# Performance work log

Measured on AMD Instinct MI355X. Metric: run time of the kernel, lower is better.

Reference implementation:

```python
import jax, jax.numpy as jnp
import numpy as np

B = 65536
NE = 256   # n_encode
NH = 256   # n_hidden
NC = 4     # n_command
D = 64     # n_depth (BatchNorm channels)
F = 32     # n_features
M = D * (F // 2)  # 1024
EPS = 1e-5


def setup_inputs() -> dict:
    key = jax.random.key(0)
    ks = jax.random.split(key, 8)
    s = 0.05
    return {
        "feature": jax.random.normal(ks[0], (B, NE), jnp.float32),
        "hidden":  jax.random.normal(ks[1], (B, NH), jnp.float32),
        "command": jax.random.normal(ks[2], (B, NC), jnp.float32),
        # linear weights (torch Linear stores [out, in]); xavier-like scale
        "Wq":  jax.random.normal(ks[3], (D, NC), jnp.float32) * s,
        "Wkz": jax.random.normal(ks[4], (M, NE), jnp.float32) * s,
        "Wkh": jax.random.normal(ks[5], (M, NH), jnp.float32) * s,
        "Wvz": jax.random.normal(ks[6], (M, NE), jnp.float32) * s,
        "Wvh": jax.random.normal(ks[7], (M, NH), jnp.float32) * s,
        # BatchNorm1d(64) affine params (normV exists in __init__ but is unused)
        "gammaQ": jnp.ones((D,), jnp.float32),
        "betaQ":  jnp.zeros((D,), jnp.float32),
        "gammaK": jnp.ones((D,), jnp.float32),
        "betaK":  jnp.zeros((D,), jnp.float32),
    }


def reference(feature, hidden, command, Wq, Wkz, Wkh, Wvz, Wvh,
              gammaQ, betaQ, gammaK, betaK):
    # Q projection: [B, D]; BatchNorm1d over batch (training-mode batch stats,
    # biased variance, matching torch).
    Q = command @ Wq.T
    mQ = jnp.mean(Q, axis=0)
    vQ = jnp.mean(jnp.square(Q - mQ), axis=0)
    Qn = (Q - mQ) / jnp.sqrt(vQ + EPS) * gammaQ + betaQ          # [B, D]

    # K: cat([B,M],[B,M]) -> [B, 2M] -> view [B, F, D] -> transpose -> [B, D, F]
    K = jnp.concatenate([feature @ Wkz.T, hidden @ Wkh.T], axis=1)
    K = K.reshape(-1, F, D).transpose(0, 2, 1)                    # [B, D, F]
    mK = jnp.mean(K, axis=(0, 2), keepdims=True)
    vK = jnp.mean(jnp.square(K - mK), axis=(0, 2), keepdims=True)
    Kn = (K - mK) / jnp.sqrt(vK + EPS) * gammaK[None, :, None] + betaK[None, :, None]

    # V: [B, F, D], NOT batch-normed (normV is dead code in the original)
    V = jnp.concatenate([feature @ Wvz.T, hidden @ Wvh.T], axis=1).reshape(-1, F, D)

    # attention: [B,1,D] @ [B,D,F] -> [B,F] scores; softmax over F; then @ V
    A = jax.nn.softmax(jnp.einsum('bd,bdf->bf', Qn, Kn) / np.sqrt(D).astype(np.float32), axis=-1)
    s = jnp.einsum('bf,bfd->bd', A, V)                            # [B, D]
    return s
```

## Files before the change

kernel.cpp:

```cpp
#include <hip/hip_runtime.h>
#include <hip/hip_bf16.h>
#include <math.h>


typedef float  f32x4   __attribute__((ext_vector_type(4)));
typedef float  f32x16  __attribute__((ext_vector_type(16)));
typedef __bf16 bf16x4  __attribute__((ext_vector_type(4)));
typedef __bf16 bf16x8  __attribute__((ext_vector_type(8)));

#define MFMA16(A, B, C) __builtin_amdgcn_mfma_f32_16x16x32_bf16((A), (B), (C), 0, 0, 0)
#define MFMA32(A, B, C) __builtin_amdgcn_mfma_f32_32x32x16_bf16((A), (B), (C), 0, 0, 0)

#define EPSV 1e-5f

#define WS_WV    0x000000u
#define WS_WKF   0x100000u
#define WS_G     0x120000u
#define WS_CS    0x1A0000u
#define WS_CMDP  0x1A0800u
#define WS_T     0x1A1800u
#define WS_U     0x1A3800u
#define WS_WQ2   0x1A5800u
#define WS_C0    0x1A5C00u

__device__ __forceinline__ void gl_lds16(const void* g, void* l)
{
    __builtin_amdgcn_global_load_lds(
        (const __attribute__((address_space(1))) unsigned int*)g,
        (__attribute__((address_space(3))) unsigned int*)l, 16, 0, 0);
}

__global__ __launch_bounds__(512, 2) void setup1(const float* __restrict__ feat,
        const float* __restrict__ hid, const float4* __restrict__ cmd,
        const float* __restrict__ Wvz, const float* __restrict__ Wvh,
        __bf16* __restrict__ WV, float* __restrict__ CMDP, float* __restrict__ CS,
        __bf16* __restrict__ Gp)
{
    __shared__ __bf16 T[2 * 256 * 40];
    __shared__ float sm[8][14];
    const int blk = blockIdx.x;
    const int tid = threadIdx.x;

    if (blk >= 384) {
        const int b2 = blk - 384;
        float v[14];
#pragma unroll
        for (int k = 0; k < 14; ++k) v[k] = 0.f;
#pragma unroll
        for (int i = 0; i < 4; ++i) {
            float4 c = cmd[(b2 * 4 + i) * 512 + tid];
            v[0] += c.x;  v[1] += c.y;  v[2] += c.z;  v[3] += c.w;
            v[4] += c.x*c.x; v[5] += c.x*c.y; v[6] += c.x*c.z; v[7] += c.x*c.w;
            v[8] += c.y*c.y; v[9] += c.y*c.z; v[10] += c.y*c.w;
            v[11] += c.z*c.z; v[12] += c.z*c.w; v[13] += c.w*c.w;
        }
#pragma unroll
        for (int k = 0; k < 14; ++k) {
            float s = v[k];
#pragma unroll
            for (int off = 32; off; off >>= 1) s += __shfl_xor(s, off);
            if ((tid & 63) == 0) sm[tid >> 6][k] = s;
        }
        __syncthreads();
        if (tid < 14) {
            float s = 0.f;
#pragma unroll
            for (int w = 0; w < 8; ++w) s += sm[w][tid];
            CMDP[b2 * 14 + tid] = s;
        }
        return;
    }
    if (blk >= 128) {
        int t = (blk - 128) * 512 + tid;
        int e = t * 4;
        const float* src = (e < 262144) ? (Wvz + e) : (Wvh + (e - 262144));
        float4 a = *(const float4*)src;
        bf16x4 vv = { (__bf16)a.x, (__bf16)a.y, (__bf16)a.z, (__bf16)a.w };
        *(bf16x4*)(WV + e) = vv;
        return;
    }

    const int mat  = blk >> 6;
    const int chunk = blk & 63;
    const float* X = mat ? hid : feat;
    float* cs = CS + mat * 256;
    const int k0   = chunk * 1024;
    const int wid  = tid >> 6, lane = tid & 63, quad = lane >> 4, l15 = lane & 15;
    const int c    = tid & 255;
    const int t8   = tid >> 8;

    f32x4 acc[2][16];
#pragma unroll
    for (int mt = 0; mt < 2; ++mt)
#pragma unroll
        for (int nt = 0; nt < 16; ++nt) acc[mt][nt] = (f32x4){0.f, 0.f, 0.f, 0.f};

    const float* Xc = X + (size_t)k0 * 256 + c;
    float ra[16], rb[16];
    float clsum = 0.f;

#define GRAM_LOAD(R, IT) do { \
        const float* p_ = Xc + (size_t)(IT) * 32 * 256; \
        _Pragma("unroll") \
        for (int i_ = 0; i_ < 16; ++i_) (R)[i_] = p_[(size_t)(t8 + 2 * i_) * 256]; \
    } while (0)
#define GRAM_WRITE(R, BUFO) do { \
        _Pragma("unroll") \
        for (int i_ = 0; i_ < 16; ++i_) { \
            float x_ = (R)[i_]; clsum += x_; \
            T[(BUFO) + c * 40 + t8 + 2 * i_] = (__bf16)x_; } \
    } while (0)
#define GRAM_MFMA(BUFO) do { \
        const __bf16* Tb_ = &T[(BUFO)]; \
        bf16x8 a0_ = *(const bf16x8*)&Tb_[(wid * 32 +      l15) * 40 + quad * 8]; \
        bf16x8 a1_ = *(const bf16x8*)&Tb_[(wid * 32 + 16 + l15) * 40 + quad * 8]; \
        _Pragma("unroll") \
        for (int nt_ = 0; nt_ < 16; ++nt_) { \
            bf16x8 b_ = *(const bf16x8*)&Tb_[(nt_ * 16 + l15) * 40 + quad * 8]; \
            acc[0][nt_] = MFMA16(a0_, b_, acc[0][nt_]); \
            acc[1][nt_] = MFMA16(a1_, b_, acc[1][nt_]); } \
    } while (0)

    GRAM_LOAD(ra, 0);
    GRAM_LOAD(rb, 1);
    GRAM_WRITE(ra, 0);
    GRAM_LOAD(ra, 2);
    __syncthreads();

    for (int it2 = 0; it2 < 16; ++it2) {
        GRAM_WRITE(rb, 10240);
        if (it2 < 15) GRAM_LOAD(rb, 2 * it2 + 3);
        GRAM_MFMA(0);
        __syncthreads();
        if (it2 < 15) {
            GRAM_WRITE(ra, 0);
            if (it2 < 14) GRAM_LOAD(ra, 2 * it2 + 4);
        }
        GRAM_MFMA(10240);
        __syncthreads();
    }
#undef GRAM_LOAD
#undef GRAM_WRITE
#undef GRAM_MFMA

    atomicAdd(&cs[c], clsum);
    __bf16* outp = Gp + (size_t)blk * 65536;
#pragma unroll
    for (int mt = 0; mt < 2; ++mt)
#pragma unroll
        for (int nt = 0; nt < 16; ++nt)
#pragma unroll
            for (int r = 0; r < 4; ++r) {
                int gi = wid * 32 + mt * 16 + quad * 4 + r;
                int gj = nt * 16 + l15;
                outp[gi * 256 + gj] = (__bf16)acc[mt][nt][r];
            }
}

__global__ void gram_reduce(const __bf16* __restrict__ Gp, float* __restrict__ G)
{
    int o = blockIdx.x * 256 + threadIdx.x;
    int mat = o >> 16, e = o & 65535;
    const __bf16* p = Gp + (size_t)mat * 64 * 65536 + e;
    float s = 0.f;
#pragma unroll 8
    for (int c = 0; c < 64; ++c) s += (float)p[(size_t)c * 65536];
    G[o] = s;
}

__global__ void rowstats(const float* __restrict__ Wkz, const float* __restrict__ Wkh,
        const float* __restrict__ G, const float* __restrict__ CS,
        float* __restrict__ Tout, float* __restrict__ Uout)
{
    const int blk = blockIdx.x;
    const int mat = blk >> 7, jg = blk & 127;
    const float* Wsrc = (mat ? Wkh : Wkz) + (size_t)jg * 8 * 256;
    const float* Gm = G + (size_t)mat * 65536;
    const float* cs = CS + mat * 256;
    __shared__ float wlT[256 * 8];
    __shared__ float red[4][16];
    const int tid = threadIdx.x, wid = tid >> 6, lane = tid & 63;
#pragma unroll
    for (int jj = 0; jj < 8; ++jj) wlT[tid * 8 + jj] = Wsrc[jj * 256 + tid];
    __syncthreads();
    float inner[8];
#pragma unroll
    for (int jj = 0; jj < 8; ++jj) inner[jj] = 0.f;
    for (int r = 0; r < 256; ++r) {
        float g = Gm[r * 256 + tid];
        float4 w0 = *(const float4*)&wlT[r * 8];
        float4 w1 = *(const float4*)&wlT[r * 8 + 4];
        inner[0] = fmaf(w0.x, g, inner[0]); inner[1] = fmaf(w0.y, g, inner[1]);
        inner[2] = fmaf(w0.z, g, inner[2]); inner[3] = fmaf(w0.w, g, inner[3]);
        inner[4] = fmaf(w1.x, g, inner[4]); inner[5] = fmaf(w1.y, g, inner[5]);
        inner[6] = fmaf(w1.z, g, inner[6]); inner[7] = fmaf(w1.w, g, inner[7]);
    }
    float cst = cs[tid];
#pragma unroll
    for (int jj = 0; jj < 8; ++jj) {
        float wme = wlT[tid * 8 + jj];
        float p = wme * inner[jj];
        float u = wme * cst;
#pragma unroll
        for (int off = 32; off; off >>= 1) { p += __shfl_xor(p, off); u += __shfl_xor(u, off); }
        if (lane == 0) { red[wid][jj] = p; red[wid][jj + 8] = u; }
    }
    __syncthreads();
    if (tid < 16) {
        float s = red[0][tid] + red[1][tid] + red[2][tid] + red[3][tid];
        int jj = tid & 7;
        int j = mat * 1024 + jg * 8 + jj;
        if (tid < 8) Tout[j] = s; else Uout[j] = s;
    }
}

__global__ void finalize_kernel(const float* __restrict__ Wq,
        const float* __restrict__ gQ, const float* __restrict__ bQ,
        const float* __restrict__ gK, const float* __restrict__ bK,
        const float* __restrict__ CMDP, const float* __restrict__ T,
        const float* __restrict__ U, float* __restrict__ Wq2, float* __restrict__ C0)
{
    __shared__ float s14[14];
    const int d = threadIdx.x;
    if (d < 14) {
        float s = 0.f;
        for (int b = 0; b < 32; ++b) s += CMDP[b * 14 + d];
        s14[d] = s;
    }
    __syncthreads();
    float s4[4] = { s14[0], s14[1], s14[2], s14[3] };
    float gc[4][4];
    gc[0][0] = s14[4];
    gc[0][1] = gc[1][0] = s14[5];
    gc[0][2] = gc[2][0] = s14[6];
    gc[0][3] = gc[3][0] = s14[7];
    gc[1][1] = s14[8];
    gc[1][2] = gc[2][1] = s14[9];
    gc[1][3] = gc[3][1] = s14[10];
    gc[2][2] = s14[11];
    gc[2][3] = gc[3][2] = s14[12];
    gc[3][3] = s14[13];
    float wq[4];
#pragma unroll
    for (int c = 0; c < 4; ++c) wq[c] = Wq[d * 4 + c];
    const float invB = 1.0f / 65536.0f;
    float mQ = (wq[0]*s4[0] + wq[1]*s4[1] + wq[2]*s4[2] + wq[3]*s4[3]) * invB;
    float eq2 = 0.f;
#pragma unroll
    for (int c = 0; c < 4; ++c)
#pragma unroll
        for (int c2 = 0; c2 < 4; ++c2) eq2 += wq[c] * wq[c2] * gc[c][c2];
    eq2 *= invB;
    float vQ  = eq2 - mQ * mQ;
    float aQ  = gQ[d] / sqrtf(vQ + EPSV);
    float bQv = bQ[d] - mQ * aQ;
    float S2 = 0.f, S1 = 0.f;
#pragma unroll
    for (int f = 0; f < 32; ++f) { S2 += T[f * 64 + d]; S1 += U[f * 64 + d]; }
    const float invBF = 1.0f / (65536.0f * 32.0f);
    float e2 = S2 * invBF, mK = S1 * invBF;
    float vK = e2 - mK * mK;
    float aK = gK[d] / sqrtf(vK + EPSV);
    float c1 = aQ * aK * 0.125f;
    C0[d] = bQv * aK * 0.125f;
#pragma unroll
    for (int c = 0; c < 4; ++c) Wq2[d * 4 + c] = c1 * wq[c];
}

__global__ void foldK(const float* __restrict__ Wkz, const float* __restrict__ Wkh,
                      const float* __restrict__ Wq2, const float* __restrict__ C0,
                      __bf16* __restrict__ WKF)
{
    const int blk = blockIdx.x;
    const int h = blk / 96, rr = blk % 96;
    const int k = threadIdx.x;
    float s = 0.f;
    if (rr < 80) {
        const int c = rr >> 4, fl = rr & 15;
        const float* Wsrc = (h ? Wkh : Wkz) + (size_t)fl * 64 * 256;
        for (int d = 0; d < 64; ++d) {
            float coef = (c == 0) ? C0[d] : Wq2[d * 4 + (c - 1)];
            s = fmaf(coef, Wsrc[d * 256 + k], s);
        }
    }
    WKF[(size_t)(h * 96 + rr) * 256 + k] = (__bf16)s;
}

__global__ __launch_bounds__(256, 2) void fused_attn(
        const float* __restrict__ feat, const float* __restrict__ hid,
        const float4* __restrict__ cmd, const __bf16* __restrict__ WV,
        const __bf16* __restrict__ WKF, float* __restrict__ out)
{
    __shared__ __bf16 BUF[32768];
    __shared__ __bf16 WGTs[16 * 132];
    const int tid  = threadIdx.x;
    const int wid  = tid >> 6, lane = tid & 63;
    const int l5   = lane & 31, hi = lane >> 5;
    const int fl   = l5 & 15;
    const bool low = (l5 < 16);
    const int wrow = (blockIdx.x << 7) + (wid << 5);

#define STAGE_CHUNK(SRC, DSTBASE, I) do { \
        int n_ = (wid << 1) + ((I) << 3) + hi; \
        gl_lds16((SRC) + n_ * 256 + ((l5 ^ (n_ & 31)) << 3), \
                 &BUF[(DSTBASE) + (((wid << 1) + ((I) << 3)) << 8)]); \
    } while (0)

    float l_i[16];
    f32x16 s_acc[2];
#pragma unroll
    for (int r = 0; r < 16; ++r) { l_i[r] = 0.f; s_acc[0][r] = 0.f; s_acc[1][r] = 0.f; }

    for (int h = 0; h < 2; ++h) {
        const float* X = h ? hid : feat;
        const __bf16* Wkf = WKF + ((size_t)h * 96 << 8);

        bf16x8 a2[16];
#pragma unroll
        for (int u = 0; u < 16; ++u) {
            const float* p = X + ((size_t)(wrow + l5) << 8) + u * 16 + hi * 8;
            float4 x0 = *(const float4*)p;
            float4 x1 = *(const float4*)(p + 4);
            a2[u] = (bf16x8){ (__bf16)x0.x, (__bf16)x0.y, (__bf16)x0.z, (__bf16)x0.w,
                              (__bf16)x1.x, (__bf16)x1.y, (__bf16)x1.z, (__bf16)x1.w };
        }

        __syncthreads();
#pragma unroll
        for (int i = 0; i < 12; ++i)
            STAGE_CHUNK(Wkf, 0, i);
        __syncthreads();

        f32x16 acc1[3];
#pragma unroll
        for (int nt = 0; nt < 3; ++nt)
#pragma unroll
            for (int r = 0; r < 16; ++r) acc1[nt][r] = 0.f;
        __builtin_amdgcn_s_setprio(1);
#pragma unroll
        for (int ks = 0; ks < 16; ++ks)
#pragma unroll
            for (int nt = 0; nt < 3; ++nt) {
                int n = nt * 32 + l5;
                bf16x8 b = *(const bf16x8*)&BUF[n * 256 + (((ks * 2 + hi) ^ (n & 31)) << 3)];
                acc1[nt] = MFMA32(a2[ks], b, acc1[nt]);
            }
        __builtin_amdgcn_s_setprio(0);

#pragma unroll
        for (int g = 0; g < 4; ++g) {
            bf16x4 wv4;
#pragma unroll
            for (int j = 0; j < 4; ++j) {
                const int r = g * 4 + j;
                const int row32 = j + 8 * g + 4 * hi;
                float4 cm = cmd[wrow + row32];
                float e0, e1, t0[3], t1[3];
#pragma unroll
                for (int nt = 0; nt < 3; ++nt) {
                    e0 = acc1[nt][r];
                    e1 = __shfl_xor(e0, 16);
                    t0[nt] = low ? e0 : e1;
                    t1[nt] = low ? e1 : e0;
                }
                float sc = t0[0] + cm.x * t1[0] + cm.y * t0[1]
                                 + cm.z * t1[1] + cm.w * t0[2];
                float w = __expf(sc);
                wv4[j] = (__bf16)w;
                float ws = w;
                ws += __shfl_xor(ws, 1); ws += __shfl_xor(ws, 2);
                ws += __shfl_xor(ws, 4); ws += __shfl_xor(ws, 8);
                l_i[r] += ws;
            }
            if (low) *(bf16x4*)&WGTs[fl * 132 + (wid << 5) + 8 * g + 4 * hi] = wv4;
        }

        __syncthreads();

        {
            const __bf16* base = WV + ((size_t)(h * 16) << 14);
#pragma unroll
            for (int i = 0; i < 8; ++i)
                STAGE_CHUNK(base, 0, i);
        }

        for (int f2 = 0; f2 < 16; ++f2) {
            const int bufsel = (f2 & 1) << 14;
            __syncthreads();
            if (f2 < 15) {
                const __bf16* base = WV + ((size_t)(h * 16 + f2 + 1) << 14);
                const int nsel = bufsel ^ 16384;
#pragma unroll
                for (int i = 0; i < 8; ++i)
                    STAGE_CHUNK(base, nsel, i);
            }
            __builtin_amdgcn_sched_barrier(0);
            f32x16 acc2[2];
#pragma unroll
            for (int r = 0; r < 16; ++r) { acc2[0][r] = 0.f; acc2[1][r] = 0.f; }
            __builtin_amdgcn_s_setprio(1);
#pragma unroll
            for (int ks = 0; ks < 16; ++ks)
#pragma unroll
                for (int nt = 0; nt < 2; ++nt) {
                    int n = nt * 32 + l5;
                    bf16x8 b = *(const bf16x8*)&BUF[bufsel + n * 256
                                                    + (((ks * 2 + hi) ^ (n & 31)) << 3)];
                    acc2[nt] = MFMA32(a2[ks], b, acc2[nt]);
                }
            __builtin_amdgcn_s_setprio(0);
#pragma unroll
            for (int g = 0; g < 4; ++g) {
                bf16x4 wv = *(const bf16x4*)&WGTs[f2 * 132 + (wid << 5) + 8 * g + 4 * hi];
#pragma unroll
                for (int j = 0; j < 4; ++j) {
                    float w = (float)wv[j];
                    s_acc[0][g * 4 + j] += w * acc2[0][g * 4 + j];
                    s_acc[1][g * 4 + j] += w * acc2[1][g * 4 + j];
                }
            }
        }
    }
#undef STAGE_CHUNK

#pragma unroll
    for (int g = 0; g < 4; ++g)
#pragma unroll
        for (int j = 0; j < 4; ++j) {
            const int r = g * 4 + j;
            float inv = 1.0f / l_i[r];
            size_t row = (size_t)(wrow + j + 8 * g + 4 * hi);
            out[(row << 6) + l5]      = s_acc[0][r] * inv;
            out[(row << 6) + 32 + l5] = s_acc[1][r] * inv;
        }
}

extern "C" void kernel_launch(void* const* d_in, const int* in_sizes, int n_in,
                              void* d_out, int out_size, void* d_ws, size_t ws_size,
                              hipStream_t stream)
{
    (void)in_sizes; (void)n_in; (void)out_size; (void)ws_size;
    const float* feature = (const float*)d_in[0];
    const float* hidden  = (const float*)d_in[1];
    const float* command = (const float*)d_in[2];
    const float* Wq      = (const float*)d_in[3];
    const float* Wkz     = (const float*)d_in[4];
    const float* Wkh     = (const float*)d_in[5];
    const float* Wvz     = (const float*)d_in[6];
    const float* Wvh     = (const float*)d_in[7];
    const float* gammaQ  = (const float*)d_in[8];
    const float* betaQ   = (const float*)d_in[9];
    const float* gammaK  = (const float*)d_in[10];
    const float* betaK   = (const float*)d_in[11];

    char* ws = (char*)d_ws;
    __bf16* WV   = (__bf16*)(ws + WS_WV);
    __bf16* WKF  = (__bf16*)(ws + WS_WKF);
    float*  G    = (float*)(ws + WS_G);
    float*  CS   = (float*)(ws + WS_CS);
    float*  CMDP = (float*)(ws + WS_CMDP);
    float*  Tj   = (float*)(ws + WS_T);
    float*  Uj   = (float*)(ws + WS_U);
    float*  Wq2  = (float*)(ws + WS_WQ2);
    float*  C0   = (float*)(ws + WS_C0);
    float*  outp = (float*)d_out;
    __bf16* Gp   = (__bf16*)d_out;

    hipMemsetAsync(ws + WS_CS, 0, 0x800, stream);
    setup1<<<416, 512, 0, stream>>>(feature, hidden, (const float4*)command,
                                    Wvz, Wvh, WV, CMDP, CS, Gp);
    gram_reduce<<<512, 256, 0, stream>>>(Gp, G);
    rowstats<<<256, 256, 0, stream>>>(Wkz, Wkh, G, CS, Tj, Uj);
    finalize_kernel<<<1, 64, 0, stream>>>(Wq, gammaQ, betaQ, gammaK, betaK,
                                          CMDP, Tj, Uj, Wq2, C0);
    foldK<<<192, 256, 0, stream>>>(Wkz, Wkh, Wq2, C0, WKF);
    fused_attn<<<512, 256, 0, stream>>>(feature, hidden, (const float4*)command,
                                        WV, WKF, outp);
}
```

Before: 328.8 us.

## Stream weights through uniform 16KB double-buffered LDS tiles to raise occupancy to 3 blocks

```diff
diff --git a/kernel.cpp b/kernel.cpp
--- a/kernel.cpp
+++ b/kernel.cpp
@@ -286,12 +286,12 @@
     WKF[(size_t)(h * 96 + rr) * 256 + k] = (__bf16)s;
 }
 
-__global__ __launch_bounds__(256, 2) void fused_attn(
+__global__ __launch_bounds__(256, 3) void fused_attn(
         const float* __restrict__ feat, const float* __restrict__ hid,
         const float4* __restrict__ cmd, const __bf16* __restrict__ WV,
         const __bf16* __restrict__ WKF, float* __restrict__ out)
 {
-    __shared__ __bf16 BUF[32768];
+    __shared__ __bf16 BUF[2 * 8192];
     __shared__ __bf16 WGTs[16 * 132];
     const int tid  = threadIdx.x;
     const int wid  = tid >> 6, lane = tid & 63;
@@ -302,7 +302,7 @@
 
 #define STAGE_CHUNK(SRC, DSTBASE, I) do { \
         int n_ = (wid << 1) + ((I) << 3) + hi; \
-        gl_lds16((SRC) + n_ * 256 + ((l5 ^ (n_ & 31)) << 3), \
+        gl_lds16((SRC) + n_ * 256 + ((l5 ^ n_) << 3), \
                  &BUF[(DSTBASE) + (((wid << 1) + ((I) << 3)) << 8)]); \
     } while (0)
 
@@ -313,7 +313,8 @@
 
     for (int h = 0; h < 2; ++h) {
         const float* X = h ? hid : feat;
-        const __bf16* Wkf = WKF + ((size_t)h * 96 << 8);
+        const __bf16* Wkf  = WKF + ((size_t)h * 96 << 8);
+        const __bf16* Vbase = WV + ((size_t)h << 18);
 
         bf16x8 a2[16];
 #pragma unroll
@@ -325,98 +326,86 @@
                               (__bf16)x1.x, (__bf16)x1.y, (__bf16)x1.z, (__bf16)x1.w };
         }
 
+        float sc[16];
+#pragma unroll
+        for (int r = 0; r < 16; ++r) sc[r] = 0.f;
+
         __syncthreads();
 #pragma unroll
-        for (int i = 0; i < 12; ++i)
+        for (int i = 0; i < 4; ++i)
             STAGE_CHUNK(Wkf, 0, i);
-        __syncthreads();
-
-        f32x16 acc1[3];
-#pragma unroll
-        for (int nt = 0; nt < 3; ++nt)
-#pragma unroll
-            for (int r = 0; r < 16; ++r) acc1[nt][r] = 0.f;
-        __builtin_amdgcn_s_setprio(1);
-#pragma unroll
-        for (int ks = 0; ks < 16; ++ks)
-#pragma unroll
-            for (int nt = 0; nt < 3; ++nt) {
-                int n = nt * 32 + l5;
-                bf16x8 b = *(const bf16x8*)&BUF[n * 256 + (((ks * 2 + hi) ^ (n & 31)) << 3)];
-                acc1[nt] = MFMA32(a2[ks], b, acc1[nt]);
-            }
-        __builtin_amdgcn_s_setprio(0);
-
-#pragma unroll
-        for (int g = 0; g < 4; ++g) {
-            bf16x4 wv4;
-#pragma unroll
-            for (int j = 0; j < 4; ++j) {
-                const int r = g * 4 + j;
-                const int row32 = j + 8 * g + 4 * hi;
-                float4 cm = cmd[wrow + row32];
-                float e0, e1, t0[3], t1[3];
-#pragma unroll
-                for (int nt = 0; nt < 3; ++nt) {
-                    e0 = acc1[nt][r];
-                    e1 = __shfl_xor(e0, 16);
-                    t0[nt] = low ? e0 : e1;
-                    t1[nt] = low ? e1 : e0;
-                }
-                float sc = t0[0] + cm.x * t1[0] + cm.y * t0[1]
-                                 + cm.z * t1[1] + cm.w * t0[2];
-                float w = __expf(sc);
-                wv4[j] = (__bf16)w;
-                float ws = w;
-                ws += __shfl_xor(ws, 1); ws += __shfl_xor(ws, 2);
-                ws += __shfl_xor(ws, 4); ws += __shfl_xor(ws, 8);
-                l_i[r] += ws;
-            }
-            if (low) *(bf16x4*)&WGTs[fl * 132 + (wid << 5) + 8 * g + 4 * hi] = wv4;
-        }
-
-        __syncthreads();
-
-        {
-            const __bf16* base = WV + ((size_t)(h * 16) << 14);
-#pragma unroll
-            for (int i = 0; i < 8; ++i)
-                STAGE_CHUNK(base, 0, i);
-        }
-
-        for (int f2 = 0; f2 < 16; ++f2) {
-            const int bufsel = (f2 & 1) << 14;
+
+        for (int t = 0; t < 35; ++t) {
+            const int bufsel = (t & 1) << 13;
             __syncthreads();
-            if (f2 < 15) {
-                const __bf16* base = WV + ((size_t)(h * 16 + f2 + 1) << 14);
-                const int nsel = bufsel ^ 16384;
-#pragma unroll
-                for (int i = 0; i < 8; ++i)
-                    STAGE_CHUNK(base, nsel, i);
+            if (t < 34) {
+                const __bf16* nsrc = (t < 2) ? (Wkf + ((t + 1) << 13))
+                                             : (Vbase + ((size_t)(t - 2) << 13));
+                const int nsel = bufsel ^ 8192;
+#pragma unroll
+                for (int i = 0; i < 4; ++i)
+                    STAGE_CHUNK(nsrc, nsel, i);
             }
             __builtin_amdgcn_sched_barrier(0);
-            f32x16 acc2[2];
-#pragma unroll
-            for (int r = 0; r < 16; ++r) { acc2[0][r] = 0.f; acc2[1][r] = 0.f; }
+            f32x16 acc;
+#pragma unroll
+            for (int r = 0; r < 16; ++r) acc[r] = 0.f;
             __builtin_amdgcn_s_setprio(1);
 #pragma unroll
-            for (int ks = 0; ks < 16; ++ks)
-#pragma unroll
-                for (int nt = 0; nt < 2; ++nt) {
-                    int n = nt * 32 + l5;
-                    bf16x8 b = *(const bf16x8*)&BUF[bufsel + n * 256
-                                                    + (((ks * 2 + hi) ^ (n & 31)) << 3)];
-                    acc2[nt] = MFMA32(a2[ks], b, acc2[nt]);
+            for (int ks = 0; ks < 16; ++ks) {
+                bf16x8 b = *(const bf16x8*)&BUF[bufsel + l5 * 256
+                                                + (((ks * 2 + hi) ^ l5) << 3)];
+                acc = MFMA32(a2[ks], b, acc);
+            }
+            __builtin_amdgcn_s_setprio(0);
+
+            if (t < 3) {
+#pragma unroll
+                for (int g = 0; g < 4; ++g)
+#pragma unroll
+                    for (int j = 0; j < 4; ++j) {
+                        const int r = g * 4 + j;
+                        float4 cm = cmd[wrow + j + 8 * g + 4 * hi];
+                        float e0 = acc[r];
+                        float e1 = __shfl_xor(e0, 16);
+                        float t0 = low ? e0 : e1;
+                        float t1 = low ? e1 : e0;
+                        if (t == 0)      sc[r] += t0 + cm.x * t1;
+                        else if (t == 1) sc[r] += cm.y * t0 + cm.z * t1;
+                        else             sc[r] += cm.w * t0;
+                    }
+                if (t == 2) {
+#pragma unroll
+                    for (int g = 0; g < 4; ++g) {
+                        bf16x4 wv4;
+#pragma unroll
+                        for (int j = 0; j < 4; ++j) {
+                            const int r = g * 4 + j;
+                            float w = __expf(sc[r]);
+                            wv4[j] = (__bf16)w;
+                            float ws = w;
+                            ws += __shfl_xor(ws, 1); ws += __shfl_xor(ws, 2);
+                            ws += __shfl_xor(ws, 4); ws += __shfl_xor(ws, 8);
+                            l_i[r] += ws;
+                        }
+                        if (low) *(bf16x4*)&WGTs[fl * 132 + (wid << 5)
+                                                 + 8 * g + 4 * hi] = wv4;
+                    }
                 }
-            __builtin_amdgcn_s_setprio(0);
-#pragma unroll
-            for (int g = 0; g < 4; ++g) {
-                bf16x4 wv = *(const bf16x4*)&WGTs[f2 * 132 + (wid << 5) + 8 * g + 4 * hi];
-#pragma unroll
-                for (int j = 0; j < 4; ++j) {
-                    float w = (float)wv[j];
-                    s_acc[0][g * 4 + j] += w * acc2[0][g * 4 + j];
-                    s_acc[1][g * 4 + j] += w * acc2[1][g * 4 + j];
+            } else {
+                const int v    = t - 3;
+                const int dsel = v & 1;
+                const int f2   = v >> 1;
+#pragma unroll
+                for (int g = 0; g < 4; ++g) {
+                    bf16x4 wv = *(const bf16x4*)&WGTs[f2 * 132 + (wid << 5)
+                                                      + 8 * g + 4 * hi];
+#pragma unroll
+                    for (int j = 0; j < 4; ++j) {
+                        float w = (float)wv[j];
+                        if (dsel == 0) s_acc[0][g * 4 + j] += w * acc[g * 4 + j];
+                        else           s_acc[1][g * 4 + j] += w * acc[g * 4 + j];
+                    }
                 }
             }
         }
```

Measured after the change: 619.2 us. 1.88x slower.

## Load MFMA weight operands directly from global memory instead of LDS staging

Applied to the files above, without the earlier changes.

```diff
diff --git a/kernel.cpp b/kernel.cpp
--- a/kernel.cpp
+++ b/kernel.cpp
@@ -22,13 +22,6 @@
 #define WS_U     0x1A3800u
 #define WS_WQ2   0x1A5800u
 #define WS_C0    0x1A5C00u
-
-__device__ __forceinline__ void gl_lds16(const void* g, void* l)
-{
-    __builtin_amdgcn_global_load_lds(
-        (const __attribute__((address_space(1))) unsigned int*)g,
-        (__attribute__((address_space(3))) unsigned int*)l, 16, 0, 0);
-}
 
 __global__ __launch_bounds__(512, 2) void setup1(const float* __restrict__ feat,
         const float* __restrict__ hid, const float4* __restrict__ cmd,
@@ -291,7 +284,6 @@
         const float4* __restrict__ cmd, const __bf16* __restrict__ WV,
         const __bf16* __restrict__ WKF, float* __restrict__ out)
 {
-    __shared__ __bf16 BUF[32768];
     __shared__ __bf16 WGTs[16 * 132];
     const int tid  = threadIdx.x;
     const int wid  = tid >> 6, lane = tid & 63;
@@ -300,12 +292,6 @@
     const bool low = (l5 < 16);
     const int wrow = (blockIdx.x << 7) + (wid << 5);
 
-#define STAGE_CHUNK(SRC, DSTBASE, I) do { \
-        int n_ = (wid << 1) + ((I) << 3) + hi; \
-        gl_lds16((SRC) + n_ * 256 + ((l5 ^ (n_ & 31)) << 3), \
-                 &BUF[(DSTBASE) + (((wid << 1) + ((I) << 3)) << 8)]); \
-    } while (0)
-
     float l_i[16];
     f32x16 s_acc[2];
 #pragma unroll
@@ -313,7 +299,6 @@
 
     for (int h = 0; h < 2; ++h) {
         const float* X = h ? hid : feat;
-        const __bf16* Wkf = WKF + ((size_t)h * 96 << 8);
 
         bf16x8 a2[16];
 #pragma unroll
@@ -325,11 +310,9 @@
                               (__bf16)x1.x, (__bf16)x1.y, (__bf16)x1.z, (__bf16)x1.w };
         }
 
-        __syncthreads();
-#pragma unroll
-        for (int i = 0; i < 12; ++i)
-            STAGE_CHUNK(Wkf, 0, i);
-        __syncthreads();
+        const __bf16* kp0 = WKF + (((size_t)(h * 96      + l5)) << 8) + hi * 8;
+        const __bf16* kp1 = kp0 + (32 << 8);
+        const __bf16* kp2 = kp0 + (64 << 8);
 
         f32x16 acc1[3];
 #pragma unroll
@@ -338,13 +321,11 @@
             for (int r = 0; r < 16; ++r) acc1[nt][r] = 0.f;
         __builtin_amdgcn_s_setprio(1);
 #pragma unroll
-        for (int ks = 0; ks < 16; ++ks)
-#pragma unroll
-            for (int nt = 0; nt < 3; ++nt) {
-                int n = nt * 32 + l5;
-                bf16x8 b = *(const bf16x8*)&BUF[n * 256 + (((ks * 2 + hi) ^ (n & 31)) << 3)];
-                acc1[nt] = MFMA32(a2[ks], b, acc1[nt]);
-            }
+        for (int ks = 0; ks < 16; ++ks) {
+            acc1[0] = MFMA32(a2[ks], *(const bf16x8*)(kp0 + ks * 16), acc1[0]);
+            acc1[1] = MFMA32(a2[ks], *(const bf16x8*)(kp1 + ks * 16), acc1[1]);
+            acc1[2] = MFMA32(a2[ks], *(const bf16x8*)(kp2 + ks * 16), acc1[2]);
+        }
         __builtin_amdgcn_s_setprio(0);
 
 #pragma unroll
@@ -375,39 +356,18 @@
             if (low) *(bf16x4*)&WGTs[fl * 132 + (wid << 5) + 8 * g + 4 * hi] = wv4;
         }
 
-        __syncthreads();
-
-        {
-            const __bf16* base = WV + ((size_t)(h * 16) << 14);
-#pragma unroll
-            for (int i = 0; i < 8; ++i)
-                STAGE_CHUNK(base, 0, i);
-        }
-
         for (int f2 = 0; f2 < 16; ++f2) {
-            const int bufsel = (f2 & 1) << 14;
-            __syncthreads();
-            if (f2 < 15) {
-                const __bf16* base = WV + ((size_t)(h * 16 + f2 + 1) << 14);
-                const int nsel = bufsel ^ 16384;
-#pragma unroll
-                for (int i = 0; i < 8; ++i)
-                    STAGE_CHUNK(base, nsel, i);
-            }
-            __builtin_amdgcn_sched_barrier(0);
+            const __bf16* vp0 = WV + (((size_t)(h * 1024 + f2 * 64 + l5)) << 8) + hi * 8;
+            const __bf16* vp1 = vp0 + (32 << 8);
             f32x16 acc2[2];
 #pragma unroll
             for (int r = 0; r < 16; ++r) { acc2[0][r] = 0.f; acc2[1][r] = 0.f; }
             __builtin_amdgcn_s_setprio(1);
 #pragma unroll
-            for (int ks = 0; ks < 16; ++ks)
-#pragma unroll
-                for (int nt = 0; nt < 2; ++nt) {
-                    int n = nt * 32 + l5;
-                    bf16x8 b = *(const bf16x8*)&BUF[bufsel + n * 256
-                                                    + (((ks * 2 + hi) ^ (n & 31)) << 3)];
-                    acc2[nt] = MFMA32(a2[ks], b, acc2[nt]);
-                }
+            for (int ks = 0; ks < 16; ++ks) {
+                acc2[0] = MFMA32(a2[ks], *(const bf16x8*)(vp0 + ks * 16), acc2[0]);
+                acc2[1] = MFMA32(a2[ks], *(const bf16x8*)(vp1 + ks * 16), acc2[1]);
+            }
             __builtin_amdgcn_s_setprio(0);
 #pragma unroll
             for (int g = 0; g < 4; ++g) {
@@ -421,7 +381,6 @@
             }
         }
     }
-#undef STAGE_CHUNK
 
 #pragma unroll
     for (int g = 0; g < 4; ++g)
```

New measurement: 501.2 us. +52.4%, slower.

## Fuse finalize into foldK, vectorize gram LDS writes, rework attention barriers

Applied to the files above, without the earlier changes.

```diff
diff --git a/kernel.cpp b/kernel.cpp
--- a/kernel.cpp
+++ b/kernel.cpp
@@ -20,8 +20,6 @@
 #define WS_CMDP  0x1A0800u
 #define WS_T     0x1A1800u
 #define WS_U     0x1A3800u
-#define WS_WQ2   0x1A5800u
-#define WS_C0    0x1A5C00u
 
 __device__ __forceinline__ void gl_lds16(const void* g, void* l)
 {
@@ -95,20 +93,23 @@
 #pragma unroll
         for (int nt = 0; nt < 16; ++nt) acc[mt][nt] = (f32x4){0.f, 0.f, 0.f, 0.f};
 
-    const float* Xc = X + (size_t)k0 * 256 + c;
+    const float* Xc = X + (size_t)k0 * 256 + c + (size_t)t8 * 16 * 256;
     float ra[16], rb[16];
     float clsum = 0.f;
 
 #define GRAM_LOAD(R, IT) do { \
         const float* p_ = Xc + (size_t)(IT) * 32 * 256; \
         _Pragma("unroll") \
-        for (int i_ = 0; i_ < 16; ++i_) (R)[i_] = p_[(size_t)(t8 + 2 * i_) * 256]; \
+        for (int i_ = 0; i_ < 16; ++i_) (R)[i_] = p_[(size_t)i_ * 256]; \
     } while (0)
 #define GRAM_WRITE(R, BUFO) do { \
         _Pragma("unroll") \
-        for (int i_ = 0; i_ < 16; ++i_) { \
-            float x_ = (R)[i_]; clsum += x_; \
-            T[(BUFO) + c * 40 + t8 + 2 * i_] = (__bf16)x_; } \
+        for (int i2_ = 0; i2_ < 4; ++i2_) { \
+            float x0_ = (R)[4*i2_], x1_ = (R)[4*i2_+1]; \
+            float x2_ = (R)[4*i2_+2], x3_ = (R)[4*i2_+3]; \
+            clsum += x0_ + x1_ + x2_ + x3_; \
+            bf16x4 v_ = { (__bf16)x0_, (__bf16)x1_, (__bf16)x2_, (__bf16)x3_ }; \
+            *(bf16x4*)&T[(BUFO) + c * 40 + t8 * 16 + i2_ * 4] = v_; } \
     } while (0)
 #define GRAM_MFMA(BUFO) do { \
         const __bf16* Tb_ = &T[(BUFO)]; \
@@ -214,72 +215,74 @@
     }
 }
 
-__global__ void finalize_kernel(const float* __restrict__ Wq,
-        const float* __restrict__ gQ, const float* __restrict__ bQ,
-        const float* __restrict__ gK, const float* __restrict__ bK,
-        const float* __restrict__ CMDP, const float* __restrict__ T,
-        const float* __restrict__ U, float* __restrict__ Wq2, float* __restrict__ C0)
+__global__ void foldK(const float* __restrict__ Wkz, const float* __restrict__ Wkh,
+                      const float* __restrict__ Wq,
+                      const float* __restrict__ gQ, const float* __restrict__ bQ,
+                      const float* __restrict__ gK, const float* __restrict__ bK,
+                      const float* __restrict__ CMDP, const float* __restrict__ T,
+                      const float* __restrict__ U, __bf16* __restrict__ WKF)
 {
     __shared__ float s14[14];
-    const int d = threadIdx.x;
-    if (d < 14) {
+    __shared__ float sC0[64];
+    __shared__ float sWq2[256];
+    const int tid = threadIdx.x;
+    if (tid < 14) {
         float s = 0.f;
-        for (int b = 0; b < 32; ++b) s += CMDP[b * 14 + d];
-        s14[d] = s;
+        for (int b = 0; b < 32; ++b) s += CMDP[b * 14 + tid];
+        s14[tid] = s;
     }
     __syncthreads();
-    float s4[4] = { s14[0], s14[1], s14[2], s14[3] };
-    float gc[4][4];
-    gc[0][0] = s14[4];
-    gc[0][1] = gc[1][0] = s14[5];
-    gc[0][2] = gc[2][0] = s14[6];
-    gc[0][3] = gc[3][0] = s14[7];
-    gc[1][1] = s14[8];
-    gc[1][2] = gc[2][1] = s14[9];
-    gc[1][3] = gc[3][1] = s14[10];
-    gc[2][2] = s14[11];
-    gc[2][3] = gc[3][2] = s14[12];
-    gc[3][3] = s14[13];
-    float wq[4];
-#pragma unroll
-    for (int c = 0; c < 4; ++c) wq[c] = Wq[d * 4 + c];
-    const float invB = 1.0f / 65536.0f;
-    float mQ = (wq[0]*s4[0] + wq[1]*s4[1] + wq[2]*s4[2] + wq[3]*s4[3]) * invB;
-    float eq2 = 0.f;
-#pragma unroll
-    for (int c = 0; c < 4; ++c)
-#pragma unroll
-        for (int c2 = 0; c2 < 4; ++c2) eq2 += wq[c] * wq[c2] * gc[c][c2];
-    eq2 *= invB;
-    float vQ  = eq2 - mQ * mQ;
-    float aQ  = gQ[d] / sqrtf(vQ + EPSV);
-    float bQv = bQ[d] - mQ * aQ;
-    float S2 = 0.f, S1 = 0.f;
-#pragma unroll
-    for (int f = 0; f < 32; ++f) { S2 += T[f * 64 + d]; S1 += U[f * 64 + d]; }
-    const float invBF = 1.0f / (65536.0f * 32.0f);
-    float e2 = S2 * invBF, mK = S1 * invBF;
-    float vK = e2 - mK * mK;
-    float aK = gK[d] / sqrtf(vK + EPSV);
-    float c1 = aQ * aK * 0.125f;
-    C0[d] = bQv * aK * 0.125f;
-#pragma unroll
-    for (int c = 0; c < 4; ++c) Wq2[d * 4 + c] = c1 * wq[c];
-}
-
-__global__ void foldK(const float* __restrict__ Wkz, const float* __restrict__ Wkh,
-                      const float* __restrict__ Wq2, const float* __restrict__ C0,
-                      __bf16* __restrict__ WKF)
-{
+    if (tid < 64) {
+        const int d = tid;
+        float s4[4] = { s14[0], s14[1], s14[2], s14[3] };
+        float gc[4][4];
+        gc[0][0] = s14[4];
+        gc[0][1] = gc[1][0] = s14[5];
+        gc[0][2] = gc[2][0] = s14[6];
+        gc[0][3] = gc[3][0] = s14[7];
+        gc[1][1] = s14[8];
+        gc[1][2] = gc[2][1] = s14[9];
+        gc[1][3] = gc[3][1] = s14[10];
+        gc[2][2] = s14[11];
+        gc[2][3] = gc[3][2] = s14[12];
+        gc[3][3] = s14[13];
+        float wq[4];
+#pragma unroll
+        for (int c = 0; c < 4; ++c) wq[c] = Wq[d * 4 + c];
+        const float invB = 1.0f / 65536.0f;
+        float mQ = (wq[0]*s4[0] + wq[1]*s4[1] + wq[2]*s4[2] + wq[3]*s4[3]) * invB;
+        float eq2 = 0.f;
+#pragma unroll
+        for (int c = 0; c < 4; ++c)
+#pragma unroll
+            for (int c2 = 0; c2 < 4; ++c2) eq2 += wq[c] * wq[c2] * gc[c][c2];
+        eq2 *= invB;
+        float vQ  = eq2 - mQ * mQ;
+        float aQ  = gQ[d] / sqrtf(vQ + EPSV);
+        float bQv = bQ[d] - mQ * aQ;
+        float S2 = 0.f, S1 = 0.f;
+#pragma unroll
+        for (int f = 0; f < 32; ++f) { S2 += T[f * 64 + d]; S1 += U[f * 64 + d]; }
+        const float invBF = 1.0f / (65536.0f * 32.0f);
+        float e2 = S2 * invBF, mK = S1 * invBF;
+        float vK = e2 - mK * mK;
+        float aK = gK[d] / sqrtf(vK + EPSV);
+        float c1 = aQ * aK * 0.125f;
+        sC0[d] = bQv * aK * 0.125f;
+#pragma unroll
+        for (int c = 0; c < 4; ++c) sWq2[d * 4 + c] = c1 * wq[c];
+    }
+    __syncthreads();
+
     const int blk = blockIdx.x;
     const int h = blk / 96, rr = blk % 96;
-    const int k = threadIdx.x;
+    const int k = tid;
     float s = 0.f;
     if (rr < 80) {
         const int c = rr >> 4, fl = rr & 15;
         const float* Wsrc = (h ? Wkh : Wkz) + (size_t)fl * 64 * 256;
         for (int d = 0; d < 64; ++d) {
-            float coef = (c == 0) ? C0[d] : Wq2[d * 4 + (c - 1)];
+            float coef = (c == 0) ? sC0[d] : sWq2[d * 4 + (c - 1)];
             s = fmaf(coef, Wsrc[d * 256 + k], s);
         }
     }
@@ -315,6 +318,11 @@
         const float* X = h ? hid : feat;
         const __bf16* Wkf = WKF + ((size_t)h * 96 << 8);
 
+        __syncthreads();
+#pragma unroll
+        for (int i = 0; i < 12; ++i)
+            STAGE_CHUNK(Wkf, 0, i);
+
         bf16x8 a2[16];
 #pragma unroll
         for (int u = 0; u < 16; ++u) {
@@ -324,11 +332,6 @@
             a2[u] = (bf16x8){ (__bf16)x0.x, (__bf16)x0.y, (__bf16)x0.z, (__bf16)x0.w,
                               (__bf16)x1.x, (__bf16)x1.y, (__bf16)x1.z, (__bf16)x1.w };
         }
-
-        __syncthreads();
-#pragma unroll
-        for (int i = 0; i < 12; ++i)
-            STAGE_CHUNK(Wkf, 0, i);
         __syncthreads();
 
         f32x16 acc1[3];
@@ -386,15 +389,20 @@
 
         for (int f2 = 0; f2 < 16; ++f2) {
             const int bufsel = (f2 & 1) << 14;
-            __syncthreads();
             if (f2 < 15) {
                 const __bf16* base = WV + ((size_t)(h * 16 + f2 + 1) << 14);
                 const int nsel = bufsel ^ 16384;
 #pragma unroll
                 for (int i = 0; i < 8; ++i)
                     STAGE_CHUNK(base, nsel, i);
+                asm volatile("s_waitcnt vmcnt(8)");
+            } else {
+                asm volatile("s_waitcnt vmcnt(0)");
             }
             __builtin_amdgcn_sched_barrier(0);
+            __builtin_amdgcn_s_barrier();
+            __builtin_amdgcn_sched_barrier(0);
+
             f32x16 acc2[2];
 #pragma unroll
             for (int r = 0; r < 16; ++r) { acc2[0][r] = 0.f; acc2[1][r] = 0.f; }
@@ -419,6 +427,9 @@
                     s_acc[1][g * 4 + j] += w * acc2[1][g * 4 + j];
                 }
             }
+            __builtin_amdgcn_sched_barrier(0);
+            __builtin_amdgcn_s_barrier();
+            __builtin_amdgcn_sched_barrier(0);
         }
     }
 #undef STAGE_CHUNK
@@ -461,8 +472,6 @@
     float*  CMDP = (float*)(ws + WS_CMDP);
     float*  Tj   = (float*)(ws + WS_T);
     float*  Uj   = (float*)(ws + WS_U);
-    float*  Wq2  = (float*)(ws + WS_WQ2);
-    float*  C0   = (float*)(ws + WS_C0);
     float*  outp = (float*)d_out;
     __bf16* Gp   = (__bf16*)d_out;
 
@@ -471,9 +480,8 @@
                                     Wvz, Wvh, WV, CMDP, CS, Gp);
     gram_reduce<<<512, 256, 0, stream>>>(Gp, G);
     rowstats<<<256, 256, 0, stream>>>(Wkz, Wkh, G, CS, Tj, Uj);
-    finalize_kernel<<<1, 64, 0, stream>>>(Wq, gammaQ, betaQ, gammaK, betaK,
-                                          CMDP, Tj, Uj, Wq2, C0);
-    foldK<<<192, 256, 0, stream>>>(Wkz, Wkh, Wq2, C0, WKF);
+    foldK<<<192, 256, 0, stream>>>(Wkz, Wkh, Wq, gammaQ, betaQ, gammaK, betaK,
+                                   CMDP, Tj, Uj, WKF);
     fused_attn<<<512, 256, 0, stream>>>(feature, hidden, (const float4*)command,
                                         WV, WKF, outp);
 }
```

New measurement: 322.8 us. Within noise of the previous version (-1.8%).
